# Performance work log

Hardware: AMD Instinct MI355X
Metric: run time of the kernel (lower is better)

The kernel has to match this reference:

```python
import jax, jax.numpy as jnp
import numpy as np

HEADS = 8
EPS = 1e-6
LN_EPS = 1e-5


def avg_pool(x, k):
    b, c, h, w = x.shape
    return x.reshape(b, c, h // k, k, w // k, k).mean(axis=(3, 5))


def layernorm(x, g, b):
    mu = x.mean(-1, keepdims=True)
    var = x.var(-1, keepdims=True)
    return (x - mu) / jnp.sqrt(var + LN_EPS) * g + b


def pos_embed_2d(h, w, c):
    # original calls build_2d_sincos_position_embedding(w=h, h=w): grid over (h, w), row-major flatten
    gw, gh = jnp.meshgrid(jnp.arange(h, dtype=jnp.float32),
                          jnp.arange(w, dtype=jnp.float32), indexing='ij')
    pd = c // 4
    omega = 1.0 / (10000.0 ** (jnp.arange(pd, dtype=jnp.float32) / pd))
    ow = gw.reshape(-1, 1) * omega  # (h*w, pd)
    oh = gh.reshape(-1, 1) * omega
    return jnp.concatenate([jnp.sin(ow), jnp.cos(ow), jnp.sin(oh), jnp.cos(oh)], axis=1)  # (h*w, c)


def _forward(a3, a4, q_w, q_b, q_ln_g, q_ln_b, k_w, k_b, k_ln_g, k_ln_b,
             v_w, v_b, out_w, out_b, lin1_w, lin1_b, lin2_w, lin2_b,
             n1_g, n1_b, n2_g, n2_b, idx):
    orig_a3 = a3
    if idx == 2:
        a3d = avg_pool(a3, 2)
    else:
        a3d = avg_pool(a3, 4)
        a4 = avg_pool(a4, 2)
    bs, c, h, w = a3d.shape
    L = h * w  # tgt_len == src_len (a3_down and a4 have equal spatial size)
    hd = c // HEADS

    residual = a3d.reshape(bs, c, L).transpose(0, 2, 1)  # (b, L, c)
    x3 = residual
    x4 = a4.reshape(bs, c, L).transpose(0, 2, 1)
    pos = pos_embed_2d(h, w, c)  # (L, c)
    x3 = x3 + pos[None]
    x4 = x4 + pos[None]

    Q = layernorm(x3 @ q_w + q_b, q_ln_g, q_ln_b)
    K = layernorm(x4 @ k_w + k_b, k_ln_g, k_ln_b)
    V = x4 @ v_w + v_b
    Q = jax.nn.relu(Q).reshape(bs, L, HEADS, hd).transpose(0, 2, 1, 3)  # (b,h,L,d)
    K = jax.nn.relu(K).reshape(bs, L, HEADS, hd).transpose(0, 2, 1, 3)
    V = V.reshape(bs, L, HEADS, hd).transpose(0, 2, 1, 3)

    # cosFormer position reweighting: index = pi/2 * (1..m) / m
    m = L
    wi = (np.pi / 2.0) * jnp.arange(1, m + 1, dtype=jnp.float32) / m  # (m,)
    sn = jnp.sin(wi)[None, None, :, None]
    cs = jnp.cos(wi)[None, None, :, None]
    Q_ = jnp.concatenate([Q * sn, Q * cs], axis=-1)  # (b,h,L,2d)
    K_ = jnp.concatenate([K * sn, K * cs], axis=-1)

    KV = jnp.einsum('bhld,bhlm->bhdm', K_, V)                     # (b,h,2d,d)
    Z = 1.0 / jnp.maximum(jnp.einsum('bhld,bhd->bhl', Q_, K_.sum(axis=2)), EPS)
    attn = jnp.einsum('bhld,bhdm->bhlm', Q_, KV) * Z[..., None]   # (b,h,L,d)
    attn = attn.transpose(0, 2, 1, 3).reshape(bs, L, c)

    out = attn @ out_w + out_b
    out = layernorm(out, n1_g, n1_b)     # normalize_before=False -> norm1 applied
    out = residual + out                 # dropout=0
    res2 = out
    out = jax.nn.gelu(out @ lin1_w + lin1_b, approximate=False) @ lin2_w + lin2_b
    out = layernorm(out, n2_g, n2_b)
    out = res2 + out

    a3sa = out.transpose(0, 2, 1).reshape(bs, c, h, w)
    a3sa = jax.image.resize(a3sa, orig_a3.shape, method='bilinear')  # align_corners=False
    return a3sa * orig_a3


def setup_inputs() -> dict:
    key = jax.random.key(0)
    ks = jax.random.split(key, 10)
    B, C = 16, 256
    C4 = 4 * C

    def w(k, shp):
        return jax.random.normal(k, shp, dtype=jnp.float32) * 0.02

    return {
        'a3': jax.random.normal(ks[0], (B, C, 128, 128), dtype=jnp.float32),
        'a4': jax.random.normal(ks[1], (B, C, 64, 64), dtype=jnp.float32),
        'q_w': w(ks[2], (C, C)), 'q_b': jnp.zeros((C,), jnp.float32),
        'q_ln_g': jnp.ones((C,), jnp.float32), 'q_ln_b': jnp.zeros((C,), jnp.float32),
        'k_w': w(ks[3], (C, C)), 'k_b': jnp.zeros((C,), jnp.float32),
        'k_ln_g': jnp.ones((C,), jnp.float32), 'k_ln_b': jnp.zeros((C,), jnp.float32),
        'v_w': w(ks[4], (C, C)), 'v_b': jnp.zeros((C,), jnp.float32),
        'out_w': w(ks[5], (C, C)), 'out_b': jnp.zeros((C,), jnp.float32),
        'lin1_w': w(ks[6], (C, C4)), 'lin1_b': jnp.zeros((C4,), jnp.float32),
        'lin2_w': w(ks[7], (C4, C)), 'lin2_b': jnp.zeros((C,), jnp.float32),
        'n1_g': jnp.ones((C,), jnp.float32), 'n1_b': jnp.zeros((C,), jnp.float32),
        'n2_g': jnp.ones((C,), jnp.float32), 'n2_b': jnp.zeros((C,), jnp.float32),
        'idx': 2,
    }


def reference(a3, a4, q_w, q_b, q_ln_g, q_ln_b, k_w, k_b, k_ln_g, k_ln_b,
              v_w, v_b, out_w, out_b, lin1_w, lin1_b, lin2_w, lin2_b,
              n1_g, n1_b, n2_g, n2_b, idx):
    return _forward(a3, a4, q_w, q_b, q_ln_g, q_ln_b, k_w, k_b, k_ln_g, k_ln_b,
                    v_w, v_b, out_w, out_b, lin1_w, lin1_b, lin2_w, lin2_b,
                    n1_g, n1_b, n2_g, n2_b, idx)
```

## Files before the change

### kernel.cpp

```cpp
#include <hip/hip_runtime.h>
#include <hip/hip_bf16.h>
#include <math.h>

#define HEADS 8
#define LL 4096
#define CDIM 256
#define BATCH 16
#define NROWS (BATCH*LL)

typedef __attribute__((ext_vector_type(8))) __bf16 bf16x8;
typedef __attribute__((ext_vector_type(4))) __bf16 bf16x4;
typedef __attribute__((ext_vector_type(4))) float f32x4;

__device__ inline float b2f(ushort u) {
    union { unsigned u; float f; } v; v.u = ((unsigned)u) << 16; return v.f;
}
__device__ inline ushort f2b(float f) {
    union { float f; unsigned u; } v; v.f = f;
    unsigned r = (v.u + 0x7FFF + ((v.u >> 16) & 1)) >> 16;
    return (ushort)r;
}
__device__ inline void gload16(const void* g, void* l) {
    __builtin_amdgcn_global_load_lds(
        (const __attribute__((address_space(1))) unsigned int*)g,
        (__attribute__((address_space(3))) unsigned int*)l, 16, 0, 0);
}
__device__ inline float fast_gelu(float v) {
    float u = 0.7978845608028654f * v * (1.0f + 0.044715f * v * v);
    float e = exp2f(u * 2.885390081777927f);
    float t = 1.0f - 2.0f / (e + 1.0f);
    return 0.5f * v * (1.0f + t);
}

__global__ __launch_bounds__(256) void prep_kernel(
    float* __restrict__ pos, float* __restrict__ snc,
    const float* __restrict__ q_w, const float* __restrict__ k_w,
    const float* __restrict__ v_w, const float* __restrict__ o_w,
    const float* __restrict__ w1, const float* __restrict__ w2,
    ushort* __restrict__ wqT, ushort* __restrict__ wkT,
    ushort* __restrict__ wvT, ushort* __restrict__ woT,
    ushort* __restrict__ w1T, ushort* __restrict__ w2T,
    float* __restrict__ ksglob)
{
    __shared__ float t[32][33];
    int bid = blockIdx.x;
    int tid = threadIdx.x;
    if (bid == 1792) {
        for (int i = tid; i < BATCH * 2 * 256; i += 256) ksglob[i] = 0.0f;
        return;
    }
    if (bid < 1024) {
        int c = tid;
        int k = c & 63;
        float omega = expf(-(float)k * (9.210340371976184f / 64.0f));
        #pragma unroll
        for (int i = 0; i < 4; ++i) {
            int l = bid * 4 + i;
            int y = l >> 6, x = l & 63;
            float coord = (c < 128) ? (float)y : (float)x;
            float ang = coord * omega;
            float val = ((c & 127) < 64) ? sinf(ang) : cosf(ang);
            pos[l * CDIM + c] = val;
            if (c < 2) {
                float wi = 1.5707963267948966f * (float)(l + 1) / (float)LL;
                snc[l * 2 + c] = (c == 0) ? sinf(wi) : cosf(wi);
            }
        }
        return;
    }
    int id = bid - 1024;
    const float* W; ushort* Wt; int K, N, kb, nb;
    if (id < 64)       { W = q_w; Wt = wqT; K = 256;  N = 256;  kb = (id & 7) * 32;  nb = (id >> 3) * 32; }
    else if (id < 128) { id -= 64;  W = k_w; Wt = wkT; K = 256;  N = 256;  kb = (id & 7) * 32;  nb = (id >> 3) * 32; }
    else if (id < 192) { id -= 128; W = v_w; Wt = wvT; K = 256;  N = 256;  kb = (id & 7) * 32;  nb = (id >> 3) * 32; }
    else if (id < 256) { id -= 192; W = o_w; Wt = woT; K = 256;  N = 256;  kb = (id & 7) * 32;  nb = (id >> 3) * 32; }
    else if (id < 512) { id -= 256; W = w1;  Wt = w1T; K = 256;  N = 1024; kb = (id & 7) * 32;  nb = (id >> 3) * 32; }
    else               { id -= 512; W = w2;  Wt = w2T; K = 1024; N = 256;  kb = (id & 31) * 32; nb = (id >> 5) * 32; }
    int x = tid & 31, y = tid >> 5;
    #pragma unroll
    for (int i = 0; i < 4; ++i)
        t[y + i * 8][x] = W[(size_t)(kb + y + i * 8) * N + nb + x];
    __syncthreads();
    #pragma unroll
    for (int i = 0; i < 4; ++i) {
        int n = y + i * 8;
        Wt[(size_t)(nb + n) * K + kb + x] = f2b(t[x][n]);
    }
}

__global__ __launch_bounds__(256) void pool_x3_kernel(
    const float* __restrict__ a3, ushort* __restrict__ residual,
    ushort* __restrict__ x3b, const float* __restrict__ pos)
{
    __shared__ float raw[64][128];
    __shared__ float pooled[64][65];
    int i = blockIdx.x, ct = blockIdx.y, b = blockIdx.z;
    int tid = threadIdx.x;
    #pragma unroll
    for (int it = 0; it < 8; ++it) {
        int lin = (it * 256 + tid) * 4;
        int x = lin & 127;
        int cc = lin >> 7;
        size_t base = ((size_t)(b * 256 + ct * 64 + cc) * 128 + 2 * i) * 128 + x;
        float4 v0 = *(const float4*)&a3[base];
        float4 v1 = *(const float4*)&a3[base + 128];
        float4 s = make_float4(v0.x + v1.x, v0.y + v1.y, v0.z + v1.z, v0.w + v1.w);
        *(float4*)&raw[cc][x] = s;
    }
    __syncthreads();
    #pragma unroll
    for (int it = 0; it < 16; ++it) {
        int idx = it * 256 + tid;
        int j = idx & 63, cc = idx >> 6;
        pooled[cc][j] = 0.25f * (raw[cc][2 * j] + raw[cc][2 * j + 1]);
    }
    __syncthreads();
    #pragma unroll
    for (int it = 0; it < 16; ++it) {
        int cc = tid & 63;
        int jj = (tid >> 6) + it * 4;
        float val = pooled[cc][jj];
        int l = i * 64 + jj;
        int c = ct * 64 + cc;
        size_t o = (size_t)(b * LL + l) * CDIM + c;
        residual[o] = f2b(val);
        x3b[o] = f2b(val + pos[l * CDIM + c]);
    }
}

__global__ __launch_bounds__(256) void x4_kernel(
    const float* __restrict__ a4, ushort* __restrict__ x4b, const float* __restrict__ pos)
{
    __shared__ float t2[64][65];
    int y = blockIdx.x, ct = blockIdx.y, b = blockIdx.z, tid = threadIdx.x;
    #pragma unroll
    for (int it = 0; it < 16; ++it) {
        int idx = it * 256 + tid;
        int x = idx & 63, cc = idx >> 6;
        t2[cc][x] = a4[((size_t)(b * 256 + ct * 64 + cc) * 64 + y) * 64 + x];
    }
    __syncthreads();
    #pragma unroll
    for (int it = 0; it < 16; ++it) {
        int cc = tid & 63;
        int xx = (tid >> 6) + it * 4;
        int l = y * 64 + xx, c = ct * 64 + cc;
        x4b[(size_t)(b * LL + l) * CDIM + c] = f2b(t2[cc][xx] + pos[l * CDIM + c]);
    }
}

template<bool DO_LN, bool DO_RELU, bool DO_RES>
__global__ __launch_bounds__(512, 4) void gemm_mfma(
    const ushort* __restrict__ A, const ushort* __restrict__ Wt,
    const float* __restrict__ bias, const float* __restrict__ gam_,
    const float* __restrict__ bet_, const ushort* __restrict__ res,
    ushort* __restrict__ outb)
{
    __shared__ ushort As[2][128 * 32];
    __shared__ ushort Bs[2][256 * 32];
    __shared__ float redS[128][4];
    __shared__ float redQ[128][4];
    __shared__ float2 mustd[128];

    const int tid = threadIdx.x;
    const int lane = tid & 63;
    const int wv = tid >> 6;
    const int wr = wv >> 2;
    const int wc = wv & 3;
    const int wvu = __builtin_amdgcn_readfirstlane(wv);
    const int row0 = blockIdx.x * 128;

    const int sr = tid >> 2;
    const int sg = (tid & 3) ^ ((sr >> 1) & 3);
    const ushort* aSrc = A + (size_t)(row0 + sr) * 256 + sg * 8;
    const ushort* bSrc0 = Wt + (size_t)sr * 256 + sg * 8;
    const ushort* bSrc1 = Wt + (size_t)(128 + sr) * 256 + sg * 8;

    const int frSlot = (lane >> 4) ^ (((lane & 15) >> 1) & 3);

    f32x4 acc[4][4] = {};
    gload16(aSrc, (char*)&As[0][0] + wvu * 1024);
    gload16(bSrc0, (char*)&Bs[0][0] + wvu * 1024);
    gload16(bSrc1, (char*)&Bs[0][0] + 8192 + wvu * 1024);
    __syncthreads();

    int cur = 0;
    for (int t = 0; t < 8; ++t) {
        if (t < 7) {
            gload16(aSrc + (t + 1) * 32, (char*)&As[cur ^ 1][0] + wvu * 1024);
            gload16(bSrc0 + (t + 1) * 32, (char*)&Bs[cur ^ 1][0] + wvu * 1024);
            gload16(bSrc1 + (t + 1) * 32, (char*)&Bs[cur ^ 1][0] + 8192 + wvu * 1024);
        }
        bf16x8 af[4], bfr[4];
        #pragma unroll
        for (int f = 0; f < 4; ++f) {
            int r = wr * 64 + f * 16 + (lane & 15);
            af[f] = *(const bf16x8*)&As[cur][r * 32 + frSlot * 8];
            int c = wc * 64 + f * 16 + (lane & 15);
            bfr[f] = *(const bf16x8*)&Bs[cur][c * 32 + frSlot * 8];
        }
        #pragma unroll
        for (int fi = 0; fi < 4; ++fi)
            #pragma unroll
            for (int fj = 0; fj < 4; ++fj)
                acc[fi][fj] = __builtin_amdgcn_mfma_f32_16x16x32_bf16(
                    af[fi], bfr[fj], acc[fi][fj], 0, 0, 0);
        __syncthreads();
        cur ^= 1;
    }

    const int cl = lane & 15;
    const int rg = lane >> 4;
    float bia[4], gmv[4], btv[4];
    #pragma unroll
    for (int fj = 0; fj < 4; ++fj) {
        int col = wc * 64 + fj * 16 + cl;
        bia[fj] = bias[col];
        if constexpr (DO_LN) { gmv[fj] = gam_[col]; btv[fj] = bet_[col]; }
    }
    #pragma unroll
    for (int fi = 0; fi < 4; ++fi)
        #pragma unroll
        for (int fj = 0; fj < 4; ++fj)
            #pragma unroll
            for (int j = 0; j < 4; ++j)
                acc[fi][fj][j] += bia[fj];

    if constexpr (DO_LN) {
        #pragma unroll
        for (int fi = 0; fi < 4; ++fi)
            #pragma unroll
            for (int j = 0; j < 4; ++j) {
                float s = acc[fi][0][j] + acc[fi][1][j] + acc[fi][2][j] + acc[fi][3][j];
                float q = acc[fi][0][j] * acc[fi][0][j] + acc[fi][1][j] * acc[fi][1][j]
                        + acc[fi][2][j] * acc[fi][2][j] + acc[fi][3][j] * acc[fi][3][j];
                #pragma unroll
                for (int m = 1; m <= 8; m <<= 1) {
                    s += __shfl_xor(s, m, 64);
                    q += __shfl_xor(q, m, 64);
                }
                if (cl == 0) {
                    int tr = wr * 64 + fi * 16 + rg * 4 + j;
                    redS[tr][wc] = s; redQ[tr][wc] = q;
                }
            }
        __syncthreads();
        if (tid < 128) {
            float s = redS[tid][0] + redS[tid][1] + redS[tid][2] + redS[tid][3];
            float q = redQ[tid][0] + redQ[tid][1] + redQ[tid][2] + redQ[tid][3];
            float mu = s * (1.0f / 256.0f);
            float var = q * (1.0f / 256.0f) - mu * mu;
            mustd[tid] = make_float2(mu, rsqrtf(var + 1e-5f));
        }
        __syncthreads();
        #pragma unroll
        for (int fi = 0; fi < 4; ++fi)
            #pragma unroll
            for (int j = 0; j < 4; ++j) {
                float2 ms = mustd[wr * 64 + fi * 16 + rg * 4 + j];
                #pragma unroll
                for (int fj = 0; fj < 4; ++fj)
                    acc[fi][fj][j] = (acc[fi][fj][j] - ms.x) * ms.y * gmv[fj] + btv[fj];
            }
    }
    if constexpr (DO_RELU) {
        #pragma unroll
        for (int fi = 0; fi < 4; ++fi)
            #pragma unroll
            for (int fj = 0; fj < 4; ++fj)
                #pragma unroll
                for (int j = 0; j < 4; ++j)
                    acc[fi][fj][j] = fmaxf(acc[fi][fj][j], 0.0f);
    }
    #pragma unroll
    for (int fi = 0; fi < 4; ++fi)
        #pragma unroll
        for (int j = 0; j < 4; ++j) {
            size_t row = row0 + wr * 64 + fi * 16 + rg * 4 + j;
            size_t rbase = row * 256 + wc * 64 + cl;
            #pragma unroll
            for (int fj = 0; fj < 4; ++fj) {
                float v = acc[fi][fj][j];
                if constexpr (DO_RES) v += b2f(res[rbase + fj * 16]);
                outb[rbase + fj * 16] = f2b(v);
            }
        }
}

__global__ __launch_bounds__(512, 2) void gemm_kv(
    const ushort* __restrict__ A, const ushort* __restrict__ wkT,
    const ushort* __restrict__ wvT, const float* __restrict__ k_b,
    const float* __restrict__ k_g, const float* __restrict__ k_beta,
    const float* __restrict__ v_b, const float* __restrict__ snc,
    float* __restrict__ ksglob, ushort* __restrict__ Kb, ushort* __restrict__ Vb)
{
    __shared__ ushort As[2][128 * 32];
    __shared__ ushort BsK[2][256 * 32];
    __shared__ ushort BsV[2][256 * 32];
    __shared__ float redS[128][4];
    __shared__ float redQ[128][4];
    __shared__ float2 mustd[128];

    const int tid = threadIdx.x;
    const int lane = tid & 63;
    const int wv = tid >> 6;
    const int wr = wv >> 2;
    const int wc = wv & 3;
    const int wvu = __builtin_amdgcn_readfirstlane(wv);
    const int row0 = blockIdx.x * 128;

    const int sr = tid >> 2;
    const int sg = (tid & 3) ^ ((sr >> 1) & 3);
    const ushort* aSrc = A + (size_t)(row0 + sr) * 256 + sg * 8;
    const ushort* bkSrc0 = wkT + (size_t)sr * 256 + sg * 8;
    const ushort* bkSrc1 = wkT + (size_t)(128 + sr) * 256 + sg * 8;
    const ushort* bvSrc0 = wvT + (size_t)sr * 256 + sg * 8;
    const ushort* bvSrc1 = wvT + (size_t)(128 + sr) * 256 + sg * 8;

    const int frSlot = (lane >> 4) ^ (((lane & 15) >> 1) & 3);

    f32x4 accK[4][4] = {};
    f32x4 accV[4][4] = {};
    gload16(aSrc, (char*)&As[0][0] + wvu * 1024);
    gload16(bkSrc0, (char*)&BsK[0][0] + wvu * 1024);
    gload16(bkSrc1, (char*)&BsK[0][0] + 8192 + wvu * 1024);
    gload16(bvSrc0, (char*)&BsV[0][0] + wvu * 1024);
    gload16(bvSrc1, (char*)&BsV[0][0] + 8192 + wvu * 1024);
    __syncthreads();

    int cur = 0;
    for (int t = 0; t < 8; ++t) {
        if (t < 7) {
            gload16(aSrc + (t + 1) * 32, (char*)&As[cur ^ 1][0] + wvu * 1024);
            gload16(bkSrc0 + (t + 1) * 32, (char*)&BsK[cur ^ 1][0] + wvu * 1024);
            gload16(bkSrc1 + (t + 1) * 32, (char*)&BsK[cur ^ 1][0] + 8192 + wvu * 1024);
            gload16(bvSrc0 + (t + 1) * 32, (char*)&BsV[cur ^ 1][0] + wvu * 1024);
            gload16(bvSrc1 + (t + 1) * 32, (char*)&BsV[cur ^ 1][0] + 8192 + wvu * 1024);
        }
        bf16x8 af[4], bk[4], bv[4];
        #pragma unroll
        for (int f = 0; f < 4; ++f) {
            int r = wr * 64 + f * 16 + (lane & 15);
            af[f] = *(const bf16x8*)&As[cur][r * 32 + frSlot * 8];
            int c = wc * 64 + f * 16 + (lane & 15);
            bk[f] = *(const bf16x8*)&BsK[cur][c * 32 + frSlot * 8];
            bv[f] = *(const bf16x8*)&BsV[cur][c * 32 + frSlot * 8];
        }
        #pragma unroll
        for (int fi = 0; fi < 4; ++fi)
            #pragma unroll
            for (int fj = 0; fj < 4; ++fj) {
                accK[fi][fj] = __builtin_amdgcn_mfma_f32_16x16x32_bf16(
                    af[fi], bk[fj], accK[fi][fj], 0, 0, 0);
                accV[fi][fj] = __builtin_amdgcn_mfma_f32_16x16x32_bf16(
                    af[fi], bv[fj], accV[fi][fj], 0, 0, 0);
            }
        __syncthreads();
        cur ^= 1;
    }

    const int cl = lane & 15;
    const int rg = lane >> 4;
    #pragma unroll
    for (int fj = 0; fj < 4; ++fj) {
        float bv_ = v_b[wc * 64 + fj * 16 + cl];
        #pragma unroll
        for (int fi = 0; fi < 4; ++fi)
            #pragma unroll
            for (int j = 0; j < 4; ++j)
                accV[fi][fj][j] += bv_;
    }
    #pragma unroll
    for (int fi = 0; fi < 4; ++fi)
        #pragma unroll
        for (int j = 0; j < 4; ++j) {
            size_t rbase = (size_t)(row0 + wr * 64 + fi * 16 + rg * 4 + j) * 256 + wc * 64 + cl;
            #pragma unroll
            for (int fj = 0; fj < 4; ++fj)
                Vb[rbase + fj * 16] = f2b(accV[fi][fj][j]);
        }
    float bia[4], gmv[4], btv[4];
    #pragma unroll
    for (int fj = 0; fj < 4; ++fj) {
        int col = wc * 64 + fj * 16 + cl;
        bia[fj] = k_b[col]; gmv[fj] = k_g[col]; btv[fj] = k_beta[col];
    }
    #pragma unroll
    for (int fi = 0; fi < 4; ++fi)
        #pragma unroll
        for (int fj = 0; fj < 4; ++fj)
            #pragma unroll
            for (int j = 0; j < 4; ++j)
                accK[fi][fj][j] += bia[fj];
    #pragma unroll
    for (int fi = 0; fi < 4; ++fi)
        #pragma unroll
        for (int j = 0; j < 4; ++j) {
            float s = accK[fi][0][j] + accK[fi][1][j] + accK[fi][2][j] + accK[fi][3][j];
            float q = accK[fi][0][j] * accK[fi][0][j] + accK[fi][1][j] * accK[fi][1][j]
                    + accK[fi][2][j] * accK[fi][2][j] + accK[fi][3][j] * accK[fi][3][j];
            #pragma unroll
            for (int m = 1; m <= 8; m <<= 1) {
                s += __shfl_xor(s, m, 64);
                q += __shfl_xor(q, m, 64);
            }
            if (cl == 0) {
                int tr = wr * 64 + fi * 16 + rg * 4 + j;
                redS[tr][wc] = s; redQ[tr][wc] = q;
            }
        }
    __syncthreads();
    if (tid < 128) {
        float s = redS[tid][0] + redS[tid][1] + redS[tid][2] + redS[tid][3];
        float q = redQ[tid][0] + redQ[tid][1] + redQ[tid][2] + redQ[tid][3];
        float mu = s * (1.0f / 256.0f);
        float var = q * (1.0f / 256.0f) - mu * mu;
        mustd[tid] = make_float2(mu, rsqrtf(var + 1e-5f));
    }
    __syncthreads();
    float kss[4] = {}, ksc[4] = {};
    #pragma unroll
    for (int fi = 0; fi < 4; ++fi)
        #pragma unroll
        for (int j = 0; j < 4; ++j) {
            int rloc = wr * 64 + fi * 16 + rg * 4 + j;
            float2 ms = mustd[rloc];
            int l = (row0 + rloc) & (LL - 1);
            float sn = snc[l * 2], cs = snc[l * 2 + 1];
            size_t rbase = (size_t)(row0 + rloc) * 256 + wc * 64 + cl;
            #pragma unroll
            for (int fj = 0; fj < 4; ++fj) {
                float v = (accK[fi][fj][j] - ms.x) * ms.y * gmv[fj] + btv[fj];
                v = fmaxf(v, 0.0f);
                Kb[rbase + fj * 16] = f2b(v);
                kss[fj] += sn * v;
                ksc[fj] += cs * v;
            }
        }
    int b = row0 >> 12;
    #pragma unroll
    for (int fj = 0; fj < 4; ++fj) {
        float s = kss[fj], c = ksc[fj];
        s += __shfl_xor(s, 16, 64); s += __shfl_xor(s, 32, 64);
        c += __shfl_xor(c, 16, 64); c += __shfl_xor(c, 32, 64);
        if (rg == 0) {
            int col = wc * 64 + fj * 16 + cl;
            atomicAdd(&ksglob[((size_t)b * 2 + 0) * 256 + col], s);
            atomicAdd(&ksglob[((size_t)b * 2 + 1) * 256 + col], c);
        }
    }
}

__global__ __launch_bounds__(256, 2) void mlp_fused(
    const ushort* __restrict__ res2, const ushort* __restrict__ w1T,
    const ushort* __restrict__ w2T, const float* __restrict__ b1,
    const float* __restrict__ b2, const float* __restrict__ gam_,
    const float* __restrict__ bet_, ushort* __restrict__ outb)
{
    __shared__ ushort As[2][64 * 32];
    __shared__ ushort Bs[2][256 * 32];
    __shared__ ushort h1c[8 * 64 * 36];
    __shared__ float redS[64][4];
    __shared__ float redQ[64][4];
    __shared__ float2 mustd[64];

    const int tid = threadIdx.x;
    const int lane = tid & 63;
    const int wv = tid >> 6;
    const int wvu = __builtin_amdgcn_readfirstlane(wv);
    const int row0 = blockIdx.x * 64;
    const int sr = tid >> 2;
    const int sg = (tid & 3) ^ ((sr >> 1) & 3);
    const ushort* aSrc = res2 + (size_t)(row0 + sr) * 256 + sg * 8;
    const int frSlot = (lane >> 4) ^ (((lane & 15) >> 1) & 3);
    const int cl = lane & 15;
    const int rg = lane >> 4;

    f32x4 acc2[4][4] = {};
    gload16(aSrc, (char*)&As[0][0] + wvu * 1024);
    #pragma unroll
    for (int j = 0; j < 4; ++j)
        gload16(w1T + (size_t)(j * 64 + sr) * 256 + sg * 8,
                (char*)&Bs[0][0] + j * 4096 + wvu * 1024);
    __syncthreads();
    int cur = 0;

    for (int c = 0; c < 4; ++c) {
        const ushort* b1Src = w1T + (size_t)(c * 256 + sr) * 256 + sg * 8;
        const ushort* b2Src = w2T + (size_t)sr * 1024 + c * 256 + sg * 8;
        f32x4 acc1[4][4] = {};
        for (int t = 0; t < 8; ++t) {
            if (t < 7) {
                gload16(aSrc + (t + 1) * 32, (char*)&As[cur ^ 1][0] + wvu * 1024);
                #pragma unroll
                for (int j = 0; j < 4; ++j)
                    gload16(b1Src + j * 64 * 256 + (t + 1) * 32,
                            (char*)&Bs[cur ^ 1][0] + j * 4096 + wvu * 1024);
            } else {
                gload16(aSrc, (char*)&As[cur ^ 1][0] + wvu * 1024);
                #pragma unroll
                for (int j = 0; j < 4; ++j)
                    gload16(b2Src + (size_t)j * 64 * 1024,
                            (char*)&Bs[cur ^ 1][0] + j * 4096 + wvu * 1024);
            }
            bf16x8 af[4], bfr[4];
            #pragma unroll
            for (int f = 0; f < 4; ++f) {
                int r = f * 16 + (lane & 15);
                af[f] = *(const bf16x8*)&As[cur][r * 32 + frSlot * 8];
                int cc2 = wv * 64 + f * 16 + (lane & 15);
                bfr[f] = *(const bf16x8*)&Bs[cur][cc2 * 32 + frSlot * 8];
            }
            #pragma unroll
            for (int fi = 0; fi < 4; ++fi)
                #pragma unroll
                for (int fj = 0; fj < 4; ++fj)
                    acc1[fi][fj] = __builtin_amdgcn_mfma_f32_16x16x32_bf16(
                        af[fi], bfr[fj], acc1[fi][fj], 0, 0, 0);
            __syncthreads();
            cur ^= 1;
        }
        float bia1[4];
        #pragma unroll
        for (int fj = 0; fj < 4; ++fj)
            bia1[fj] = b1[c * 256 + wv * 64 + fj * 16 + cl];
        #pragma unroll
        for (int fi = 0; fi < 4; ++fi)
            #pragma unroll
            for (int fj = 0; fj < 4; ++fj) {
                int tch = wv * 2 + (fj >> 1);
                int kk_local = (fj & 1) * 16 + cl;
                #pragma unroll
                for (int j = 0; j < 4; ++j) {
                    float v = acc1[fi][fj][j] + bia1[fj];
                    float g = fast_gelu(v);
                    int row = fi * 16 + rg * 4 + j;
                    h1c[tch * 2304 + row * 36 + kk_local] = f2b(g);
                }
            }
        __syncthreads();
        for (int t = 0; t < 8; ++t) {
            if (t < 7) {
                #pragma unroll
                for (int j = 0; j < 4; ++j)
                    gload16(b2Src + (size_t)j * 64 * 1024 + (t + 1) * 32,
                            (char*)&Bs[cur ^ 1][0] + j * 4096 + wvu * 1024);
            } else {
                int cn = (c < 3) ? c + 1 : 3;
                #pragma unroll
                for (int j = 0; j < 4; ++j)
                    gload16(w1T + (size_t)(cn * 256 + j * 64 + sr) * 256 + sg * 8,
                            (char*)&Bs[cur ^ 1][0] + j * 4096 + wvu * 1024);
            }
            bf16x8 af[4], bfr[4];
            #pragma unroll
            for (int f = 0; f < 4; ++f) {
                int r = f * 16 + (lane & 15);
                int ho = t * 2304 + r * 36 + (lane >> 4) * 8;
                bf16x4 lo = *(const bf16x4*)&h1c[ho];
                bf16x4 hi = *(const bf16x4*)&h1c[ho + 4];
                bf16x8 a_;
                a_[0] = lo[0]; a_[1] = lo[1]; a_[2] = lo[2]; a_[3] = lo[3];
                a_[4] = hi[0]; a_[5] = hi[1]; a_[6] = hi[2]; a_[7] = hi[3];
                af[f] = a_;
                int cc2 = wv * 64 + f * 16 + (lane & 15);
                bfr[f] = *(const bf16x8*)&Bs[cur][cc2 * 32 + frSlot * 8];
            }
            #pragma unroll
            for (int fi = 0; fi < 4; ++fi)
                #pragma unroll
                for (int fj = 0; fj < 4; ++fj)
                    acc2[fi][fj] = __builtin_amdgcn_mfma_f32_16x16x32_bf16(
                        af[fi], bfr[fj], acc2[fi][fj], 0, 0, 0);
            __syncthreads();
            cur ^= 1;
        }
    }
    float bia[4], gmv[4], btv[4];
    #pragma unroll
    for (int fj = 0; fj < 4; ++fj) {
        int col = wv * 64 + fj * 16 + cl;
        bia[fj] = b2[col];
        gmv[fj] = gam_[col];
        btv[fj] = bet_[col];
    }
    #pragma unroll
    for (int fi = 0; fi < 4; ++fi)
        #pragma unroll
        for (int fj = 0; fj < 4; ++fj)
            #pragma unroll
            for (int j = 0; j < 4; ++j)
                acc2[fi][fj][j] += bia[fj];
    #pragma unroll
    for (int fi = 0; fi < 4; ++fi)
        #pragma unroll
        for (int j = 0; j < 4; ++j) {
            float s = acc2[fi][0][j] + acc2[fi][1][j] + acc2[fi][2][j] + acc2[fi][3][j];
            float q = acc2[fi][0][j] * acc2[fi][0][j] + acc2[fi][1][j] * acc2[fi][1][j]
                    + acc2[fi][2][j] * acc2[fi][2][j] + acc2[fi][3][j] * acc2[fi][3][j];
            #pragma unroll
            for (int m = 1; m <= 8; m <<= 1) {
                s += __shfl_xor(s, m, 64);
                q += __shfl_xor(q, m, 64);
            }
            if (cl == 0) { redS[fi * 16 + rg * 4 + j][wv] = s; redQ[fi * 16 + rg * 4 + j][wv] = q; }
        }
    __syncthreads();
    if (tid < 64) {
        float s = redS[tid][0] + redS[tid][1] + redS[tid][2] + redS[tid][3];
        float q = redQ[tid][0] + redQ[tid][1] + redQ[tid][2] + redQ[tid][3];
        float mu = s * (1.0f / 256.0f);
        float var = q * (1.0f / 256.0f) - mu * mu;
        mustd[tid] = make_float2(mu, rsqrtf(var + 1e-5f));
    }
    __syncthreads();
    #pragma unroll
    for (int fi = 0; fi < 4; ++fi)
        #pragma unroll
        for (int j = 0; j < 4; ++j) {
            float2 ms = mustd[fi * 16 + rg * 4 + j];
            size_t row = row0 + fi * 16 + rg * 4 + j;
            size_t rbase = row * 256 + wv * 64 + cl;
            #pragma unroll
            for (int fj = 0; fj < 4; ++fj) {
                float v = (acc2[fi][fj][j] - ms.x) * ms.y * gmv[fj] + btv[fj];
                v += b2f(res2[rbase + fj * 16]);
                outb[rbase + fj * 16] = f2b(v);
            }
        }
}

__global__ __launch_bounds__(256) void kv_kernel(
    const ushort* __restrict__ Kmat, const ushort* __restrict__ Vmat,
    const float* __restrict__ snc, float* __restrict__ kvpart)
{
    __shared__ float Kt[64][36];
    __shared__ float Vt[64][36];
    __shared__ float sns[64], css[64];
    int chunk = blockIdx.x;
    int bh = blockIdx.y;
    int b = bh >> 3, h = bh & 7;
    int tid = threadIdx.x;
    int m = tid & 31;
    int d0 = (tid >> 5) * 4;
    float accs[4] = {}, accc[4] = {};
    int l0chunk = chunk * 512;
    int lrow = tid >> 2;
    int lcol = (tid & 3) * 8;
    for (int sub = 0; sub < 8; ++sub) {
        int l0 = l0chunk + sub * 64;
        {
            size_t gbase = (size_t)(b * LL + l0 + lrow) * CDIM + h * 32 + lcol;
            uint4 kr = *(const uint4*)&Kmat[gbase];
            uint4 vr = *(const uint4*)&Vmat[gbase];
            float* kd = &Kt[lrow][lcol];
            float* vd = &Vt[lrow][lcol];
            kd[0] = b2f((ushort)(kr.x & 0xffff)); kd[1] = b2f((ushort)(kr.x >> 16));
            kd[2] = b2f((ushort)(kr.y & 0xffff)); kd[3] = b2f((ushort)(kr.y >> 16));
            kd[4] = b2f((ushort)(kr.z & 0xffff)); kd[5] = b2f((ushort)(kr.z >> 16));
            kd[6] = b2f((ushort)(kr.w & 0xffff)); kd[7] = b2f((ushort)(kr.w >> 16));
            vd[0] = b2f((ushort)(vr.x & 0xffff)); vd[1] = b2f((ushort)(vr.x >> 16));
            vd[2] = b2f((ushort)(vr.y & 0xffff)); vd[3] = b2f((ushort)(vr.y >> 16));
            vd[4] = b2f((ushort)(vr.z & 0xffff)); vd[5] = b2f((ushort)(vr.z >> 16));
            vd[6] = b2f((ushort)(vr.w & 0xffff)); vd[7] = b2f((ushort)(vr.w >> 16));
        }
        if (tid < 64) { sns[tid] = snc[(l0 + tid) * 2]; css[tid] = snc[(l0 + tid) * 2 + 1]; }
        __syncthreads();
        #pragma unroll 4
        for (int lt = 0; lt < 64; ++lt) {
            float v = Vt[lt][m];
            float vs = v * sns[lt];
            float vc = v * css[lt];
            float4 kd4 = *(const float4*)&Kt[lt][d0];
            accs[0] += kd4.x * vs; accc[0] += kd4.x * vc;
            accs[1] += kd4.y * vs; accc[1] += kd4.y * vc;
            accs[2] += kd4.z * vs; accc[2] += kd4.z * vc;
            accs[3] += kd4.w * vs; accc[3] += kd4.w * vc;
        }
        __syncthreads();
    }
    size_t base = (size_t)(bh * 8 + chunk) * 2048;
    #pragma unroll
    for (int i2 = 0; i2 < 4; ++i2) {
        kvpart[base + (d0 + i2) * 32 + m] = accs[i2];
        kvpart[base + 1024 + (d0 + i2) * 32 + m] = accc[i2];
    }
}

__global__ __launch_bounds__(256) void kvred_kernel(
    const float* __restrict__ kvpart, const float* __restrict__ ksglob,
    ushort* __restrict__ Bimg)
{
    int bh = blockIdx.x;
    int b = bh >> 3, h = bh & 7;
    int tid = threadIdx.x;
    for (int e = tid; e < 2560; e += 256) {
        int n = e >> 5;
        int k = e & 31;
        int t = n >> 4, col = n & 15;
        float v = 0.0f;
        if (t < 4) {
            int off = (t >= 2 ? 1024 : 0) + k * 32 + (t & 1) * 16 + col;
            #pragma unroll
            for (int ch = 0; ch < 8; ++ch)
                v += kvpart[(size_t)(bh * 8 + ch) * 2048 + off];
        } else if (col < 2) {
            v = ksglob[((size_t)b * 2 + col) * 256 + h * 32 + k];
        }
        ushort hi = f2b(v);
        ushort lo = f2b(v - b2f(hi));
        Bimg[(size_t)bh * 5120 + n * 32 + k] = hi;
        Bimg[(size_t)bh * 5120 + (80 + n) * 32 + k] = lo;
    }
}

__global__ __launch_bounds__(256, 2) void attn_mfma(
    const ushort* __restrict__ Qmat, const ushort* __restrict__ Bimg,
    const float* __restrict__ snc, ushort* __restrict__ attnOut)
{
    __shared__ ushort Bs[5120];
    int ltile = blockIdx.x, h = blockIdx.y, b = blockIdx.z;
    int bh = b * 8 + h;
    int tid = threadIdx.x;
    int lane = tid & 63;
    int wv = tid >> 6;

    for (int e = tid; e < 640; e += 256)
        *(uint4*)&Bs[e * 8] = *(const uint4*)&Bimg[(size_t)bh * 5120 + e * 8];
    __syncthreads();

    bf16x8 bfr[10];
    #pragma unroll
    for (int tt = 0; tt < 10; ++tt) {
        int row = (tt < 5 ? tt * 16 : 80 + (tt - 5) * 16) + (lane & 15);
        bfr[tt] = *(const bf16x8*)&Bs[row * 32 + (lane >> 4) * 8];
    }
    int lbase = ltile * 256 + wv * 64;
    bf16x8 af[4];
    #pragma unroll
    for (int fi = 0; fi < 4; ++fi) {
        int l = lbase + fi * 16 + (lane & 15);
        af[fi] = *(const bf16x8*)&Qmat[(size_t)(b * LL + l) * CDIM + h * 32 + (lane >> 4) * 8];
    }
    f32x4 acc[4][5] = {};
    #pragma unroll
    for (int fi = 0; fi < 4; ++fi)
        #pragma unroll
        for (int t = 0; t < 5; ++t) {
            acc[fi][t] = __builtin_amdgcn_mfma_f32_16x16x32_bf16(af[fi], bfr[t], acc[fi][t], 0, 0, 0);
            acc[fi][t] = __builtin_amdgcn_mfma_f32_16x16x32_bf16(af[fi], bfr[t + 5], acc[fi][t], 0, 0, 0);
        }

    int zlane = lane & 48;
    int cl = lane & 15;
    #pragma unroll
    for (int fi = 0; fi < 4; ++fi) {
        #pragma unroll
        for (int j = 0; j < 4; ++j) {
            float zraw = acc[fi][4][j];
            float zs = __shfl(zraw, zlane, 64);
            float zc = __shfl(zraw, zlane | 1, 64);
            int l = lbase + fi * 16 + ((lane >> 4) & 3) * 4 + j;
            float sn = snc[l * 2], cs = snc[l * 2 + 1];
            float den = sn * zs + cs * zc;
            float Z = 1.0f / fmaxf(den, 1e-6f);
            float v0 = (sn * acc[fi][0][j] + cs * acc[fi][2][j]) * Z;
            float v1 = (sn * acc[fi][1][j] + cs * acc[fi][3][j]) * Z;
            size_t ob = (size_t)(b * LL + l) * CDIM + h * 32 + cl;
            attnOut[ob] = f2b(v0);
            attnOut[ob + 16] = f2b(v1);
        }
    }
}

__global__ __launch_bounds__(256) void resize_mul_kernel(
    const ushort* __restrict__ ffeat, const float* __restrict__ a3, float* __restrict__ out)
{
    __shared__ float ft[3][64][65];
    int k = blockIdx.x, ct = blockIdx.y, b = blockIdx.z;
    int tid = threadIdx.x;
    for (int it = 0; it < 48; ++it) {
        int e = it * 256 + tid;
        int cc = e & 63;
        int xs = (e >> 6) & 63;
        int ys = e >> 12;
        int ysrc = min(max(k - 1 + ys, 0), 63);
        ft[ys][cc][xs] = b2f(ffeat[(size_t)(b * LL + ysrc * 64 + xs) * CDIM + ct * 64 + cc]);
    }
    __syncthreads();
    int x = tid & 127;
    int half = tid >> 7;
    int y = 2 * k + half;
    int ysA, ysB; float wyA, wyB;
    if (half == 0) { ysA = 0; ysB = 1; wyA = 0.25f; wyB = 0.75f; }
    else           { ysA = 1; ysB = 2; wyA = 0.75f; wyB = 0.25f; }
    int x0; float wx1;
    if ((x & 1) == 0) { x0 = x / 2 - 1; wx1 = 0.75f; }
    else              { x0 = x / 2;     wx1 = 0.25f; }
    int x0c = max(x0, 0);
    int x1c = min(x0 + 1, 63);
    float wx0 = 1.0f - wx1;
    for (int cc = 0; cc < 64; ++cc) {
        float rA = wx0 * ft[ysA][cc][x0c] + wx1 * ft[ysA][cc][x1c];
        float rB = wx0 * ft[ysB][cc][x0c] + wx1 * ft[ysB][cc][x1c];
        float val = wyA * rA + wyB * rB;
        size_t oidx = ((size_t)(b * 256 + ct * 64 + cc) * 128 + y) * 128 + x;
        out[oidx] = val * a3[oidx];
    }
}

extern "C" void kernel_launch(void* const* d_in, const int* in_sizes, int n_in,
                              void* d_out, int out_size, void* d_ws, size_t ws_size,
                              hipStream_t stream)
{
    const float* a3     = (const float*)d_in[0];
    const float* a4     = (const float*)d_in[1];
    const float* q_w    = (const float*)d_in[2];
    const float* q_b    = (const float*)d_in[3];
    const float* q_ln_g = (const float*)d_in[4];
    const float* q_ln_b = (const float*)d_in[5];
    const float* k_w    = (const float*)d_in[6];
    const float* k_b    = (const float*)d_in[7];
    const float* k_ln_g = (const float*)d_in[8];
    const float* k_ln_b = (const float*)d_in[9];
    const float* v_w    = (const float*)d_in[10];
    const float* v_b    = (const float*)d_in[11];
    const float* out_w  = (const float*)d_in[12];
    const float* out_b  = (const float*)d_in[13];
    const float* lin1_w = (const float*)d_in[14];
    const float* lin1_b = (const float*)d_in[15];
    const float* lin2_w = (const float*)d_in[16];
    const float* lin2_b = (const float*)d_in[17];
    const float* n1_g   = (const float*)d_in[18];
    const float* n1_b   = (const float*)d_in[19];
    const float* n2_g   = (const float*)d_in[20];
    const float* n2_b   = (const float*)d_in[21];
    float* out = (float*)d_out;
    char* base = (char*)d_ws;

    const size_t MiB = 1024 * 1024;
    float*  pos      = (float*)(base);
    float*  snc      = (float*)(base + 4 * MiB);
    ushort* wqT      = (ushort*)(base + 4 * MiB + 64 * 1024);
    ushort* wkT      = wqT + 256 * 256;
    ushort* wvT      = wkT + 256 * 256;
    ushort* woT      = wvT + 256 * 256;
    ushort* w1T      = woT + 256 * 256;
    ushort* w2T      = w1T + 1024 * 256;
    ushort* residual = (ushort*)(base + 6 * MiB);
    ushort* x3b      = (ushort*)(base + 38 * MiB);
    ushort* x4b      = (ushort*)(base + 70 * MiB);
    ushort* Qb       = (ushort*)(base + 102 * MiB);
    ushort* Kb       = (ushort*)(base + 134 * MiB);
    ushort* Vb       = (ushort*)(base + 166 * MiB);
    float*  kvp      = (float*)(base + 198 * MiB);
    float*  ksglob   = (float*)(base + 206 * MiB);
    ushort* Bimg     = (ushort*)(base + 207 * MiB);
    ushort* attnb    = x3b;
    ushort* res2b    = x4b;
    ushort* ffeat    = residual;

    prep_kernel<<<1793, 256, 0, stream>>>(pos, snc, q_w, k_w, v_w, out_w, lin1_w, lin2_w,
                                          wqT, wkT, wvT, woT, w1T, w2T, ksglob);
    pool_x3_kernel<<<dim3(64, 4, 16), 256, 0, stream>>>(a3, residual, x3b, pos);
    x4_kernel<<<dim3(64, 4, 16), 256, 0, stream>>>(a4, x4b, pos);

    gemm_mfma<true, true, false><<<NROWS / 128, 512, 0, stream>>>(
        x3b, wqT, q_b, q_ln_g, q_ln_b, nullptr, Qb);
    gemm_kv<<<NROWS / 128, 512, 0, stream>>>(
        x4b, wkT, wvT, k_b, k_ln_g, k_ln_b, v_b, snc, ksglob, Kb, Vb);

    kv_kernel<<<dim3(8, 128), 256, 0, stream>>>(Kb, Vb, snc, kvp);
    kvred_kernel<<<128, 256, 0, stream>>>(kvp, ksglob, Bimg);
    attn_mfma<<<dim3(16, 8, 16), 256, 0, stream>>>(Qb, Bimg, snc, attnb);

    gemm_mfma<true, false, true><<<NROWS / 128, 512, 0, stream>>>(
        attnb, woT, out_b, n1_g, n1_b, residual, res2b);
    mlp_fused<<<NROWS / 64, 256, 0, stream>>>(
        res2b, w1T, w2T, lin1_b, lin2_b, n2_g, n2_b, ffeat);

    resize_mul_kernel<<<dim3(64, 4, 16), 256, 0, stream>>>(ffeat, a3, out);
}
```

Before: 549.6 us.

## Triple-buffer GEMM K-loop with vmcnt waits and enlarge MLP tile to 128 rows

Replaces the double-buffered global-to-LDS pipeline in the Q, KV, out-proj and MLP GEMMs with a three-stage ring that prefetches two K-steps ahead. Each step waits with explicit s_waitcnt vmcnt and a single barrier, where before it did a full __syncthreads after every step. The fused MLP kernel also moves from 64-row/256-thread blocks to 128-row/512-thread blocks with a 2x4 wave grid, so each weight tile is reused across twice as many rows. In exchange, LDS use rises substantially, especially the h1c buffer in mlp_fused, which may cut occupancy. Correctness now depends on the vmcnt counts matching the number of loads issued per stage.

After: 551.5 us. About the same (+0.3%).

```diff
diff --git a/kernel.cpp b/kernel.cpp
--- a/kernel.cpp
+++ b/kernel.cpp
@@ -24,6 +24,9 @@
     __builtin_amdgcn_global_load_lds(
         (const __attribute__((address_space(1))) unsigned int*)g,
         (__attribute__((address_space(3))) unsigned int*)l, 16, 0, 0);
+}
+template<int N> __device__ inline void wait_vmcnt() {
+    asm volatile("s_waitcnt vmcnt(%0)" :: "n"(N) : "memory");
 }
 __device__ inline float fast_gelu(float v) {
     float u = 0.7978845608028654f * v * (1.0f + 0.044715f * v * v);
@@ -156,8 +159,8 @@
     const float* __restrict__ bet_, const ushort* __restrict__ res,
     ushort* __restrict__ outb)
 {
-    __shared__ ushort As[2][128 * 32];
-    __shared__ ushort Bs[2][256 * 32];
+    __shared__ ushort As[3][128 * 32];
+    __shared__ ushort Bs[3][256 * 32];
     __shared__ float redS[128][4];
     __shared__ float redQ[128][4];
     __shared__ float2 mustd[128];
@@ -178,26 +181,27 @@
 
     const int frSlot = (lane >> 4) ^ (((lane & 15) >> 1) & 3);
 
+    auto issue = [&](int t, int buf) {
+        gload16(aSrc + t * 32, (char*)&As[buf][0] + wvu * 1024);
+        gload16(bSrc0 + t * 32, (char*)&Bs[buf][0] + wvu * 1024);
+        gload16(bSrc1 + t * 32, (char*)&Bs[buf][0] + 8192 + wvu * 1024);
+    };
+
     f32x4 acc[4][4] = {};
-    gload16(aSrc, (char*)&As[0][0] + wvu * 1024);
-    gload16(bSrc0, (char*)&Bs[0][0] + wvu * 1024);
-    gload16(bSrc1, (char*)&Bs[0][0] + 8192 + wvu * 1024);
-    __syncthreads();
-
-    int cur = 0;
+    issue(0, 0); issue(1, 1);
+    #pragma unroll
     for (int t = 0; t < 8; ++t) {
-        if (t < 7) {
-            gload16(aSrc + (t + 1) * 32, (char*)&As[cur ^ 1][0] + wvu * 1024);
-            gload16(bSrc0 + (t + 1) * 32, (char*)&Bs[cur ^ 1][0] + wvu * 1024);
-            gload16(bSrc1 + (t + 1) * 32, (char*)&Bs[cur ^ 1][0] + 8192 + wvu * 1024);
-        }
+        if (t < 7) wait_vmcnt<3>(); else wait_vmcnt<0>();
+        __builtin_amdgcn_s_barrier();
+        if (t + 2 < 8) issue(t + 2, (t + 2) % 3);
+        const int cb = t % 3;
         bf16x8 af[4], bfr[4];
         #pragma unroll
         for (int f = 0; f < 4; ++f) {
             int r = wr * 64 + f * 16 + (lane & 15);
-            af[f] = *(const bf16x8*)&As[cur][r * 32 + frSlot * 8];
+            af[f] = *(const bf16x8*)&As[cb][r * 32 + frSlot * 8];
             int c = wc * 64 + f * 16 + (lane & 15);
-            bfr[f] = *(const bf16x8*)&Bs[cur][c * 32 + frSlot * 8];
+            bfr[f] = *(const bf16x8*)&Bs[cb][c * 32 + frSlot * 8];
         }
         #pragma unroll
         for (int fi = 0; fi < 4; ++fi)
@@ -205,9 +209,8 @@
             for (int fj = 0; fj < 4; ++fj)
                 acc[fi][fj] = __builtin_amdgcn_mfma_f32_16x16x32_bf16(
                     af[fi], bfr[fj], acc[fi][fj], 0, 0, 0);
-        __syncthreads();
-        cur ^= 1;
-    }
+    }
+    __syncthreads();
 
     const int cl = lane & 15;
     const int rg = lane >> 4;
@@ -294,9 +297,9 @@
     const float* __restrict__ v_b, const float* __restrict__ snc,
     float* __restrict__ ksglob, ushort* __restrict__ Kb, ushort* __restrict__ Vb)
 {
-    __shared__ ushort As[2][128 * 32];
-    __shared__ ushort BsK[2][256 * 32];
-    __shared__ ushort BsV[2][256 * 32];
+    __shared__ ushort As[3][128 * 32];
+    __shared__ ushort BsK[3][256 * 32];
+    __shared__ ushort BsV[3][256 * 32];
     __shared__ float redS[128][4];
     __shared__ float redQ[128][4];
     __shared__ float2 mustd[128];
@@ -319,32 +322,31 @@
 
     const int frSlot = (lane >> 4) ^ (((lane & 15) >> 1) & 3);
 
+    auto issue = [&](int t, int buf) {
+        gload16(aSrc + t * 32, (char*)&As[buf][0] + wvu * 1024);
+        gload16(bkSrc0 + t * 32, (char*)&BsK[buf][0] + wvu * 1024);
+        gload16(bkSrc1 + t * 32, (char*)&BsK[buf][0] + 8192 + wvu * 1024);
+        gload16(bvSrc0 + t * 32, (char*)&BsV[buf][0] + wvu * 1024);
+        gload16(bvSrc1 + t * 32, (char*)&BsV[buf][0] + 8192 + wvu * 1024);
+    };
+
     f32x4 accK[4][4] = {};
     f32x4 accV[4][4] = {};
-    gload16(aSrc, (char*)&As[0][0] + wvu * 1024);
-    gload16(bkSrc0, (char*)&BsK[0][0] + wvu * 1024);
-    gload16(bkSrc1, (char*)&BsK[0][0] + 8192 + wvu * 1024);
-    gload16(bvSrc0, (char*)&BsV[0][0] + wvu * 1024);
-    gload16(bvSrc1, (char*)&BsV[0][0] + 8192 + wvu * 1024);
-    __syncthreads();
-
-    int cur = 0;
+    issue(0, 0); issue(1, 1);
+    #pragma unroll
     for (int t = 0; t < 8; ++t) {
-        if (t < 7) {
-            gload16(aSrc + (t + 1) * 32, (char*)&As[cur ^ 1][0] + wvu * 1024);
-            gload16(bkSrc0 + (t + 1) * 32, (char*)&BsK[cur ^ 1][0] + wvu * 1024);
-            gload16(bkSrc1 + (t + 1) * 32, (char*)&BsK[cur ^ 1][0] + 8192 + wvu * 1024);
-            gload16(bvSrc0 + (t + 1) * 32, (char*)&BsV[cur ^ 1][0] + wvu * 1024);
-            gload16(bvSrc1 + (t + 1) * 32, (char*)&BsV[cur ^ 1][0] + 8192 + wvu * 1024);
-        }
+        if (t < 7) wait_vmcnt<5>(); else wait_vmcnt<0>();
+        __builtin_amdgcn_s_barrier();
+        if (t + 2 < 8) issue(t + 2, (t + 2) % 3);
+        const int cb = t % 3;
         bf16x8 af[4], bk[4], bv[4];
         #pragma unroll
         for (int f = 0; f < 4; ++f) {
             int r = wr * 64 + f * 16 + (lane & 15);
-            af[f] = *(const bf16x8*)&As[cur][r * 32 + frSlot * 8];
+            af[f] = *(const bf16x8*)&As[cb][r * 32 + frSlot * 8];
             int c = wc * 64 + f * 16 + (lane & 15);
-            bk[f] = *(const bf16x8*)&BsK[cur][c * 32 + frSlot * 8];
-            bv[f] = *(const bf16x8*)&BsV[cur][c * 32 + frSlot * 8];
+            bk[f] = *(const bf16x8*)&BsK[cb][c * 32 + frSlot * 8];
+            bv[f] = *(const bf16x8*)&BsV[cb][c * 32 + frSlot * 8];
         }
         #pragma unroll
         for (int fi = 0; fi < 4; ++fi)
@@ -355,9 +357,8 @@
                 accV[fi][fj] = __builtin_amdgcn_mfma_f32_16x16x32_bf16(
                     af[fi], bv[fj], accV[fi][fj], 0, 0, 0);
             }
-        __syncthreads();
-        cur ^= 1;
-    }
+    }
+    __syncthreads();
 
     const int cl = lane & 15;
     const int rg = lane >> 4;
@@ -451,24 +452,26 @@
     }
 }
 
-__global__ __launch_bounds__(256, 2) void mlp_fused(
+__global__ __launch_bounds__(512, 2) void mlp_fused(
     const ushort* __restrict__ res2, const ushort* __restrict__ w1T,
     const ushort* __restrict__ w2T, const float* __restrict__ b1,
     const float* __restrict__ b2, const float* __restrict__ gam_,
     const float* __restrict__ bet_, ushort* __restrict__ outb)
 {
-    __shared__ ushort As[2][64 * 32];
-    __shared__ ushort Bs[2][256 * 32];
-    __shared__ ushort h1c[8 * 64 * 36];
-    __shared__ float redS[64][4];
-    __shared__ float redQ[64][4];
-    __shared__ float2 mustd[64];
+    __shared__ ushort As[3][128 * 32];
+    __shared__ ushort Bs[3][256 * 32];
+    __shared__ ushort h1c[8 * 128 * 36];
+    __shared__ float redS[128][4];
+    __shared__ float redQ[128][4];
+    __shared__ float2 mustd[128];
 
     const int tid = threadIdx.x;
     const int lane = tid & 63;
     const int wv = tid >> 6;
+    const int wr = wv >> 2;
+    const int wc = wv & 3;
     const int wvu = __builtin_amdgcn_readfirstlane(wv);
-    const int row0 = blockIdx.x * 64;
+    const int row0 = blockIdx.x * 128;
     const int sr = tid >> 2;
     const int sg = (tid & 3) ^ ((sr >> 1) & 3);
     const ushort* aSrc = res2 + (size_t)(row0 + sr) * 256 + sg * 8;
@@ -477,39 +480,37 @@
     const int rg = lane >> 4;
 
     f32x4 acc2[4][4] = {};
-    gload16(aSrc, (char*)&As[0][0] + wvu * 1024);
-    #pragma unroll
-    for (int j = 0; j < 4; ++j)
-        gload16(w1T + (size_t)(j * 64 + sr) * 256 + sg * 8,
-                (char*)&Bs[0][0] + j * 4096 + wvu * 1024);
-    __syncthreads();
-    int cur = 0;
-
     for (int c = 0; c < 4; ++c) {
-        const ushort* b1Src = w1T + (size_t)(c * 256 + sr) * 256 + sg * 8;
-        const ushort* b2Src = w2T + (size_t)sr * 1024 + c * 256 + sg * 8;
+        const ushort* b1Src0 = w1T + (size_t)(c * 256 + sr) * 256 + sg * 8;
+        const ushort* b1Src1 = w1T + (size_t)(c * 256 + 128 + sr) * 256 + sg * 8;
+        const ushort* b2Src0 = w2T + (size_t)sr * 1024 + c * 256 + sg * 8;
+        const ushort* b2Src1 = w2T + (size_t)(128 + sr) * 1024 + c * 256 + sg * 8;
+
+        auto issue1 = [&](int t, int buf) {
+            gload16(aSrc + t * 32, (char*)&As[buf][0] + wvu * 1024);
+            gload16(b1Src0 + t * 32, (char*)&Bs[buf][0] + wvu * 1024);
+            gload16(b1Src1 + t * 32, (char*)&Bs[buf][0] + 8192 + wvu * 1024);
+        };
+        auto issue2 = [&](int t, int buf) {
+            gload16(b2Src0 + t * 32, (char*)&Bs[buf][0] + wvu * 1024);
+            gload16(b2Src1 + t * 32, (char*)&Bs[buf][0] + 8192 + wvu * 1024);
+        };
+
         f32x4 acc1[4][4] = {};
+        issue1(0, 0); issue1(1, 1);
+        #pragma unroll
         for (int t = 0; t < 8; ++t) {
-            if (t < 7) {
-                gload16(aSrc + (t + 1) * 32, (char*)&As[cur ^ 1][0] + wvu * 1024);
-                #pragma unroll
-                for (int j = 0; j < 4; ++j)
-                    gload16(b1Src + j * 64 * 256 + (t + 1) * 32,
-                            (char*)&Bs[cur ^ 1][0] + j * 4096 + wvu * 1024);
-            } else {
-                gload16(aSrc, (char*)&As[cur ^ 1][0] + wvu * 1024);
-                #pragma unroll
-                for (int j = 0; j < 4; ++j)
-                    gload16(b2Src + (size_t)j * 64 * 1024,
-                            (char*)&Bs[cur ^ 1][0] + j * 4096 + wvu * 1024);
-            }
+            if (t < 7) wait_vmcnt<3>(); else wait_vmcnt<0>();
+            __builtin_amdgcn_s_barrier();
+            if (t + 2 < 8) issue1(t + 2, (t + 2) % 3);
+            const int cb = t % 3;
             bf16x8 af[4], bfr[4];
             #pragma unroll
             for (int f = 0; f < 4; ++f) {
-                int r = f * 16 + (lane & 15);
-                af[f] = *(const bf16x8*)&As[cur][r * 32 + frSlot * 8];
-                int cc2 = wv * 64 + f * 16 + (lane & 15);
-                bfr[f] = *(const bf16x8*)&Bs[cur][cc2 * 32 + frSlot * 8];
+                int r = wr * 64 + f * 16 + (lane & 15);
+                af[f] = *(const bf16x8*)&As[cb][r * 32 + frSlot * 8];
+                int cc2 = wc * 64 + f * 16 + (lane & 15);
+                bfr[f] = *(const bf16x8*)&Bs[cb][cc2 * 32 + frSlot * 8];
             }
             #pragma unroll
             for (int fi = 0; fi < 4; ++fi)
@@ -517,54 +518,46 @@
                 for (int fj = 0; fj < 4; ++fj)
                     acc1[fi][fj] = __builtin_amdgcn_mfma_f32_16x16x32_bf16(
                         af[fi], bfr[fj], acc1[fi][fj], 0, 0, 0);
-            __syncthreads();
-            cur ^= 1;
         }
         float bia1[4];
         #pragma unroll
         for (int fj = 0; fj < 4; ++fj)
-            bia1[fj] = b1[c * 256 + wv * 64 + fj * 16 + cl];
+            bia1[fj] = b1[c * 256 + wc * 64 + fj * 16 + cl];
         #pragma unroll
         for (int fi = 0; fi < 4; ++fi)
             #pragma unroll
             for (int fj = 0; fj < 4; ++fj) {
-                int tch = wv * 2 + (fj >> 1);
+                int tch = wc * 2 + (fj >> 1);
                 int kk_local = (fj & 1) * 16 + cl;
                 #pragma unroll
                 for (int j = 0; j < 4; ++j) {
                     float v = acc1[fi][fj][j] + bia1[fj];
                     float g = fast_gelu(v);
-                    int row = fi * 16 + rg * 4 + j;
-                    h1c[tch * 2304 + row * 36 + kk_local] = f2b(g);
+                    int row = wr * 64 + fi * 16 + rg * 4 + j;
+                    h1c[tch * 4608 + row * 36 + kk_local] = f2b(g);
                 }
             }
         __syncthreads();
+        issue2(0, 0); issue2(1, 1);
+        #pragma unroll
         for (int t = 0; t < 8; ++t) {
-            if (t < 7) {
-                #pragma unroll
-                for (int j = 0; j < 4; ++j)
-                    gload16(b2Src + (size_t)j * 64 * 1024 + (t + 1) * 32,
-                            (char*)&Bs[cur ^ 1][0] + j * 4096 + wvu * 1024);
-            } else {
-                int cn = (c < 3) ? c + 1 : 3;
-                #pragma unroll
-                for (int j = 0; j < 4; ++j)
-                    gload16(w1T + (size_t)(cn * 256 + j * 64 + sr) * 256 + sg * 8,
-                            (char*)&Bs[cur ^ 1][0] + j * 4096 + wvu * 1024);
-            }
+            if (t < 7) wait_vmcnt<2>(); else wait_vmcnt<0>();
+            __builtin_amdgcn_s_barrier();
+            if (t + 2 < 8) issue2(t + 2, (t + 2) % 3);
+            const int cb = t % 3;
             bf16x8 af[4], bfr[4];
             #pragma unroll
             for (int f = 0; f < 4; ++f) {
-                int r = f * 16 + (lane & 15);
-                int ho = t * 2304 + r * 36 + (lane >> 4) * 8;
+                int r = wr * 64 + f * 16 + (lane & 15);
+                int ho = t * 4608 + r * 36 + (lane >> 4) * 8;
                 bf16x4 lo = *(const bf16x4*)&h1c[ho];
                 bf16x4 hi = *(const bf16x4*)&h1c[ho + 4];
                 bf16x8 a_;
                 a_[0] = lo[0]; a_[1] = lo[1]; a_[2] = lo[2]; a_[3] = lo[3];
                 a_[4] = hi[0]; a_[5] = hi[1]; a_[6] = hi[2]; a_[7] = hi[3];
                 af[f] = a_;
-                int cc2 = wv * 64 + f * 16 + (lane & 15);
-                bfr[f] = *(const bf16x8*)&Bs[cur][cc2 * 32 + frSlot * 8];
+                int cc2 = wc * 64 + f * 16 + (lane & 15);
+                bfr[f] = *(const bf16x8*)&Bs[cb][cc2 * 32 + frSlot * 8];
             }
             #pragma unroll
             for (int fi = 0; fi < 4; ++fi)
@@ -572,14 +565,13 @@
                 for (int fj = 0; fj < 4; ++fj)
                     acc2[fi][fj] = __builtin_amdgcn_mfma_f32_16x16x32_bf16(
                         af[fi], bfr[fj], acc2[fi][fj], 0, 0, 0);
-            __syncthreads();
-            cur ^= 1;
-        }
+        }
+        __syncthreads();
     }
     float bia[4], gmv[4], btv[4];
     #pragma unroll
     for (int fj = 0; fj < 4; ++fj) {
-        int col = wv * 64 + fj * 16 + cl;
+        int col = wc * 64 + fj * 16 + cl;
         bia[fj] = b2[col];
         gmv[fj] = gam_[col];
         btv[fj] = bet_[col];
@@ -603,10 +595,13 @@
                 s += __shfl_xor(s, m, 64);
                 q += __shfl_xor(q, m, 64);
             }
-            if (cl == 0) { redS[fi * 16 + rg * 4 + j][wv] = s; redQ[fi * 16 + rg * 4 + j][wv] = q; }
-        }
-    __syncthreads();
-    if (tid < 64) {
+            if (cl == 0) {
+                int tr = wr * 64 + fi * 16 + rg * 4 + j;
+                redS[tr][wc] = s; redQ[tr][wc] = q;
+            }
+        }
+    __syncthreads();
+    if (tid < 128) {
         float s = redS[tid][0] + redS[tid][1] + redS[tid][2] + redS[tid][3];
         float q = redQ[tid][0] + redQ[tid][1] + redQ[tid][2] + redQ[tid][3];
         float mu = s * (1.0f / 256.0f);
@@ -618,9 +613,9 @@
     for (int fi = 0; fi < 4; ++fi)
         #pragma unroll
         for (int j = 0; j < 4; ++j) {
-            float2 ms = mustd[fi * 16 + rg * 4 + j];
-            size_t row = row0 + fi * 16 + rg * 4 + j;
-            size_t rbase = row * 256 + wv * 64 + cl;
+            float2 ms = mustd[wr * 64 + fi * 16 + rg * 4 + j];
+            size_t row = row0 + wr * 64 + fi * 16 + rg * 4 + j;
+            size_t rbase = row * 256 + wc * 64 + cl;
             #pragma unroll
             for (int fj = 0; fj < 4; ++fj) {
                 float v = (acc2[fi][fj][j] - ms.x) * ms.y * gmv[fj] + btv[fj];
@@ -876,7 +871,7 @@
 
     gemm_mfma<true, false, true><<<NROWS / 128, 512, 0, stream>>>(
         attnb, woT, out_b, n1_g, n1_b, residual, res2b);
-    mlp_fused<<<NROWS / 64, 256, 0, stream>>>(
+    mlp_fused<<<NROWS / 128, 512, 0, stream>>>(
         res2b, w1T, w2T, lin1_b, lin2_b, n2_g, n2_b, ffeat);
 
     resize_mul_kernel<<<dim3(64, 4, 16), 256, 0, stream>>>(ffeat, a3, out);
```
